# Performance work log

Hardware: AMD Instinct MI355X
Metric: run time of the kernel (lower is better)

Reference implementation:

```python
import jax, jax.numpy as jnp
import numpy as np


def _grid_neighbors(H, W):
    # 4-neighbor grid adjacency for the Mesh([H, W]) graph
    idx = np.arange(H * W).reshape(H, W)
    p = np.full((H + 2, W + 2), -1, dtype=np.int64)
    p[1:-1, 1:-1] = idx
    nbrs = np.stack([p[0:H, 1:W + 1], p[2:H + 2, 1:W + 1], p[1:H + 1, 0:W], p[1:H + 1, 2:W + 2]], axis=-1).reshape(H * W, 4)
    mask = (nbrs >= 0).astype(np.float32)
    return np.where(nbrs >= 0, nbrs, 0), mask, mask.sum(-1) + 1.0


def _conv(x, w, b):
    y = jax.lax.conv_general_dilated(x, w, (1, 1), 'SAME', dimension_numbers=('NCHW', 'OIHW', 'NCHW'))
    return y + b[None, :, None, None]


def _dconv(x, w1, b1, w2, b2):
    return jax.nn.relu(_conv(jax.nn.relu(_conv(x, w1, b1)), w2, b2))


def _maxpool(x):
    return jax.lax.reduce_window(x, -jnp.inf, jax.lax.max, (1, 1, 2, 2), (1, 1, 2, 2), 'VALID')


def _convT(x, w, b):
    # kernel=2, stride=2 transposed conv (non-overlapping upsample)
    y = jax.lax.conv_transpose(x, w, (2, 2), 'VALID', dimension_numbers=('NCHW', 'HWIO', 'NCHW'))
    return y + b[None, :, None, None]


def _gconv(X, W, b, nbrs, mask, deg):
    # mesh graph conv: D^-1 (A + I) X W, irregular gather over grid adjacency
    g = X[:, nbrs, :]                                          # [B, N, 4, C]
    agg = ((g * mask[None, :, :, None]).sum(2) + X) / deg[None, :, None]
    return jax.nn.relu(jnp.einsum('bnc,cd->bnd', agg, W) + b[None, None, :])


def _forward(x, d1w1, d1b1, d1w2, d1b2, d2w1, d2b1, d2w2, d2b2, md1w, md1b, md2w, md2b, mbw, mbb, mu1w, mu1b, mu2w, mu2b, u3tw, u3tb, u3w1, u3b1, u3w2, u3b2, u4tw, u4tb, u4w1, u4b1, u4w2, u4b2, ow, ob):
    b1 = _dconv(x, d1w1, d1b1, d1w2, d1b2)                     # [1,64,256,256]
    b2 = _dconv(_maxpool(b1), d2w1, d2b1, d2w2, d2b2)          # [1,128,128,128]
    fe = _maxpool(b2)                                           # [1,128,64,64]
    fe = jnp.pad(fe, ((0, 0), (0, 0), (1, 1), (1, 1)))          # pad -> 66x66
    B, C, Hm, Wm = fe.shape
    nbrs, mask, deg = _grid_neighbors(Hm, Wm)
    nbrs, mask, deg = jnp.asarray(nbrs), jnp.asarray(mask), jnp.asarray(deg)
    X = fe.reshape(B, C, Hm * Wm).transpose(0, 2, 1)            # [1, 4356, 128]
    bp1 = _gconv(X, md1w, md1b, nbrs, mask, deg)                # 256 (skip)
    bp2 = _gconv(bp1, md2w, md2b, nbrs, mask, deg)              # 512 (skip)
    Xb = _gconv(bp2, mbw, mbb, nbrs, mask, deg)                 # 1024 mesh bottleneck
    X = _gconv(Xb, mu1w, mu1b, nbrs, mask, deg) + bp2           # 512
    X = _gconv(X, mu2w, mu2b, nbrs, mask, deg) + bp1            # 256
    fe = X.transpose(0, 2, 1).reshape(B, 256, Hm, Wm)[:, :, 1:-1, 1:-1]  # unpad -> 64x64
    u3 = _convT(fe, u3tw, u3tb)                                 # [1,128,128,128]
    fe = _dconv(jnp.concatenate([b2, u3], 1), u3w1, u3b1, u3w2, u3b2)
    u4 = _convT(fe, u4tw, u4tb)                                 # [1,64,256,256]
    fe = _dconv(jnp.concatenate([b1, u4], 1), u4w1, u4b1, u4w2, u4b2)
    return _conv(fe, ow, ob)[:, 0]                              # [1,256,256]


def setup_inputs():
    ks = iter(jax.random.split(jax.random.key(0), 40))
    def W(shape, fan_in):
        return jax.random.normal(next(ks), shape, jnp.float32) * np.float32(np.sqrt(2.0 / fan_in))
    def Z(n):
        return jnp.zeros((n,), jnp.float32)
    return {
        'x': jax.random.normal(next(ks), (1, 3, 256, 256), jnp.float32),
        'd1w1': W((64, 3, 3, 3), 27), 'd1b1': Z(64), 'd1w2': W((64, 64, 3, 3), 576), 'd1b2': Z(64),
        'd2w1': W((128, 64, 3, 3), 576), 'd2b1': Z(128), 'd2w2': W((128, 128, 3, 3), 1152), 'd2b2': Z(128),
        'md1w': W((128, 256), 128), 'md1b': Z(256),
        'md2w': W((256, 512), 256), 'md2b': Z(512),
        'mbw': W((512, 1024), 512), 'mbb': Z(1024),
        'mu1w': W((1024, 512), 1024), 'mu1b': Z(512),
        'mu2w': W((512, 256), 512), 'mu2b': Z(256),
        'u3tw': W((2, 2, 256, 128), 1024), 'u3tb': Z(128),
        'u3w1': W((128, 256, 3, 3), 2304), 'u3b1': Z(128), 'u3w2': W((128, 128, 3, 3), 1152), 'u3b2': Z(128),
        'u4tw': W((2, 2, 128, 64), 512), 'u4tb': Z(64),
        'u4w1': W((64, 128, 3, 3), 1152), 'u4b1': Z(64), 'u4w2': W((64, 64, 3, 3), 576), 'u4b2': Z(64),
        'ow': W((1, 64, 3, 3), 576), 'ob': Z(1),
    }


def reference(x, d1w1, d1b1, d1w2, d1b2, d2w1, d2b1, d2w2, d2b2, md1w, md1b, md2w, md2b, mbw, mbb, mu1w, mu1b, mu2w, mu2b, u3tw, u3tb, u3w1, u3b1, u3w2, u3b2, u4tw, u4tb, u4w1, u4b1, u4w2, u4b2, ow, ob):
    return _forward(x, d1w1, d1b1, d1w2, d1b2, d2w1, d2b1, d2w2, d2b2, md1w, md1b, md2w, md2b, mbw, mbb, mu1w, mu1b, mu2w, mu2b, u3tw, u3tb, u3w1, u3b1, u3w2, u3b2, u4tw, u4tb, u4w1, u4b1, u4w2, u4b2, ow, ob)
```

## Files before the change

### kernel.cpp

```cpp
#include <hip/hip_runtime.h>
#include <cstddef>

#define TPB 256

typedef __attribute__((ext_vector_type(8))) short short8;
typedef __attribute__((ext_vector_type(4))) float f32x4;

__device__ inline unsigned short f2bf(float f) {
    unsigned int u = __builtin_bit_cast(unsigned int, f);
    u += 0x7fffu + ((u >> 16) & 1u);
    return (unsigned short)(u >> 16);
}
__device__ inline float bf2f(unsigned short h) {
    unsigned int u = ((unsigned int)h) << 16;
    return __builtin_bit_cast(float, u);
}

struct TapOffs { int o[9]; };

template<int KCW>
__global__ __launch_bounds__(TPB) void k_gemmS(
    const unsigned short* __restrict__ A0, const unsigned short* __restrict__ Wf,
    const float* __restrict__ bias, const unsigned short* __restrict__ resid,
    unsigned short* __restrict__ O0, int NTtot)
{
    constexpr int K = KCW * 128;
    __shared__ float red[12 * 4 * 64 * 4];
    int lane = threadIdx.x & 63, wave = threadIdx.x >> 6;
    int ml = lane & 15, kq = lane >> 4;
    int m0 = blockIdx.x * 64, nb = blockIdx.y;
    int N = NTtot * 16;

    const unsigned short* Ap[4];
    #pragma unroll
    for (int i = 0; i < 4; ++i) {
        int mf = (wave + i) & 3;
        Ap[i] = A0 + (size_t)(m0 + mf * 16 + ml) * K + wave * (KCW * 32) + kq * 8;
    }
    const unsigned short* Bp = Wf + ((size_t)(wave * KCW) * NTtot + nb * 4) * 512 + lane * 8;

    f32x4 acc[4][4];
    #pragma unroll
    for (int i = 0; i < 4; ++i)
        #pragma unroll
        for (int nt = 0; nt < 4; ++nt) acc[i][nt] = (f32x4){0.f, 0.f, 0.f, 0.f};

    #pragma unroll
    for (int q = 0; q < KCW; ++q) {
        short8 b[4];
        #pragma unroll
        for (int nt = 0; nt < 4; ++nt)
            b[nt] = *(const short8*)(Bp + ((size_t)q * NTtot + nt) * 512);
        short8 a[4];
        #pragma unroll
        for (int i = 0; i < 4; ++i)
            a[i] = *(const short8*)(Ap[i] + q * 32);
        #pragma unroll
        for (int i = 0; i < 4; ++i)
            #pragma unroll
            for (int nt = 0; nt < 4; ++nt)
                acc[i][nt] = __builtin_amdgcn_mfma_f32_16x16x32_bf16(a[i], b[nt], acc[i][nt], 0, 0, 0);
    }

    #pragma unroll
    for (int i = 1; i < 4; ++i) {
        int s = wave * 3 + (i - 1);
        #pragma unroll
        for (int nt = 0; nt < 4; ++nt)
            *(f32x4*)&red[(((s * 4 + nt) * 64) + lane) * 4] = acc[i][nt];
    }
    __syncthreads();
    #pragma unroll
    for (int w2 = 0; w2 < 4; ++w2) {
        if (w2 == wave) continue;
        int i = (wave - w2) & 3;
        int s = w2 * 3 + (i - 1);
        #pragma unroll
        for (int nt = 0; nt < 4; ++nt) {
            f32x4 v = *(const f32x4*)&red[(((s * 4 + nt) * 64) + lane) * 4];
            acc[0][nt] += v;
        }
    }

    int mrow = m0 + wave * 16 + kq * 4;
    unsigned short* Ot = O0 + (size_t)mrow * N + nb * 64;
    const unsigned short* Rt = resid ? resid + (size_t)mrow * N + nb * 64 : nullptr;
    #pragma unroll
    for (int nt = 0; nt < 4; ++nt) {
        float bv = bias[nb * 64 + nt * 16 + ml];
        #pragma unroll
        for (int r = 0; r < 4; ++r) {
            float v = fmaxf(acc[0][nt][r] + bv, 0.f);
            if (Rt) v += bf2f(Rt[(size_t)r * N + nt * 16 + ml]);
            Ot[(size_t)r * N + nt * 16 + ml] = f2bf(v);
        }
    }
}

template<int CHUNKS>
__global__ __launch_bounds__(TPB) void k_conv3g(
    const unsigned short* __restrict__ A0, const unsigned short* __restrict__ Wf,
    const float* __restrict__ bias, unsigned short* __restrict__ O0,
    int AP, int tilesX, int OMS, int OP, int NTtot)
{
    constexpr int Cs  = CHUNKS * 64;
    constexpr int KC2 = CHUNKS * 2;
    __shared__ unsigned short Bs[2][12288];

    int lane = threadIdx.x & 63, wave = threadIdx.x >> 6;
    int ml = lane & 15, kq = lane >> 4;
    int nb = blockIdx.y;
    int tileX = blockIdx.x % tilesX, tileY = blockIdx.x / tilesX;
    int gx0 = tileX * 64, gy = tileY * 4 + wave;

    const unsigned short* Abase = A0 + (size_t)(gy - 1) * AP
                                     + (size_t)(gx0 + ml - 1) * Cs + kq * 8;

    f32x4 acc[4][4];
    #pragma unroll
    for (int mf = 0; mf < 4; ++mf)
        #pragma unroll
        for (int nt = 0; nt < 4; ++nt) acc[mf][nt] = (f32x4){0.f, 0.f, 0.f, 0.f};

    const int G = CHUNKS * 3;

    auto stageB = [&](int g) {
        int ch = g / 3, ky = g - (g / 3) * 3;
        unsigned short* bd = Bs[g & 1];
        #pragma unroll
        for (int it = 0; it < 6; ++it) {
            int u = threadIdx.x + it * TPB;
            int e = u * 8;
            int kxq = e >> 11;
            int rem = e & 2047;
            int kx = kxq >> 1, q = kxq & 1;
            const unsigned short* src = Wf
                + ((size_t)((ky * 3 + kx) * KC2 + ch * 2 + q) * NTtot + nb * 4) * 512 + rem;
            *(int4*)&bd[e] = *(const int4*)src;
        }
    };

    stageB(0);
    __syncthreads();
    for (int g = 0; g < G; ++g) {
        if (g + 1 < G) stageB(g + 1);
        int ch = g / 3, ky = g - (g / 3) * 3;
        const unsigned short* Ar = Abase + (size_t)ky * AP + ch * 64;
        const unsigned short* Bb = &Bs[g & 1][lane * 8];
        #pragma unroll
        for (int kx = 0; kx < 3; ++kx) {
            #pragma unroll
            for (int q = 0; q < 2; ++q) {
                short8 b[4];
                #pragma unroll
                for (int nt = 0; nt < 4; ++nt)
                    b[nt] = *(const short8*)(Bb + (kx * 2 + q) * 2048 + nt * 512);
                short8 a[4];
                #pragma unroll
                for (int mf = 0; mf < 4; ++mf)
                    a[mf] = *(const short8*)(Ar + (size_t)(kx + mf * 16) * Cs + q * 32);
                #pragma unroll
                for (int mf = 0; mf < 4; ++mf)
                    #pragma unroll
                    for (int nt = 0; nt < 4; ++nt)
                        acc[mf][nt] = __builtin_amdgcn_mfma_f32_16x16x32_bf16(a[mf], b[nt], acc[mf][nt], 0, 0, 0);
            }
        }
        __syncthreads();
    }

    unsigned short* Orow = O0 + (size_t)gy * OP + (size_t)nb * 64;
    #pragma unroll
    for (int mf = 0; mf < 4; ++mf) {
        int gx = gx0 + mf * 16 + kq * 4;
        #pragma unroll
        for (int nt = 0; nt < 4; ++nt) {
            float bv = bias[nb * 64 + nt * 16 + ml];
            #pragma unroll
            for (int r = 0; r < 4; ++r) {
                float v = fmaxf(acc[mf][nt][r] + bv, 0.f);
                Orow[(size_t)(gx + r) * OMS + nt * 16 + ml] = f2bf(v);
            }
        }
    }
}

template<int MW, int KC>
__global__ __launch_bounds__(TPB) void k_gemm(
    const unsigned short* __restrict__ A0, const unsigned short* __restrict__ Wf,
    const float* __restrict__ bias, const unsigned short* __restrict__ resid, int RS,
    unsigned short* __restrict__ O0,
    int Cs, int AP, int Wimg, int OMS, int OP,
    int T, TapOffs toffs, int NTtot, int relu, int ct, int ctDy, int ctDx)
{
    int lane = threadIdx.x & 63, wave = threadIdx.x >> 6;
    int ml = lane & 15, kq = lane >> 4;
    int nb = blockIdx.y;

    const unsigned short* Wb = Wf;
    unsigned short* Ob = O0;
    if (ct) {
        int tp = blockIdx.z;
        Wb += (size_t)(tp * KC) * NTtot * 512;
        int dy = 1 - (tp >> 1), dx = 1 - (tp & 1);
        Ob += (size_t)dy * ctDy + (size_t)dx * ctDx;
    }
    const unsigned short* WbB = Wb + (size_t)(nb * 4) * 512 + lane * 8;

    int fy[MW], fx[MW];
    const unsigned short* Af[MW];
    #pragma unroll
    for (int f = 0; f < MW; ++f) {
        int mf = (blockIdx.x * 4 + wave) * (16 * MW) + f * 16;
        int y = mf / Wimg, x = mf - y * Wimg;
        fy[f] = y; fx[f] = x;
        Af[f] = A0 + (size_t)y * AP + (size_t)(x + ml) * Cs + kq * 8;
    }

    f32x4 acc[MW][4];
    #pragma unroll
    for (int f = 0; f < MW; ++f)
        #pragma unroll
        for (int nt = 0; nt < 4; ++nt) acc[f][nt] = (f32x4){0.f, 0.f, 0.f, 0.f};

    for (int tp = 0; tp < T; ++tp) {
        int toff = toffs.o[tp];
        const unsigned short* Wt = WbB + (size_t)(tp * KC) * NTtot * 512;
        #pragma unroll
        for (int q = 0; q < KC; ++q) {
            short8 b[4];
            #pragma unroll
            for (int nt = 0; nt < 4; ++nt)
                b[nt] = *(const short8*)(Wt + (size_t)q * NTtot * 512 + nt * 512);
            short8 a[MW];
            #pragma unroll
            for (int f = 0; f < MW; ++f)
                a[f] = *(const short8*)(Af[f] + toff + q * 32);
            #pragma unroll
            for (int f = 0; f < MW; ++f)
                #pragma unroll
                for (int nt = 0; nt < 4; ++nt)
                    acc[f][nt] = __builtin_amdgcn_mfma_f32_16x16x32_bf16(a[f], b[nt], acc[f][nt], 0, 0, 0);
        }
    }

    #pragma unroll
    for (int f = 0; f < MW; ++f) {
        unsigned short* Ot = Ob + (size_t)fy[f] * OP + (size_t)(fx[f] + kq * 4) * OMS + (size_t)nb * 64;
        int mg0 = (blockIdx.x * 4 + wave) * (16 * MW) + f * 16 + kq * 4;
        #pragma unroll
        for (int nt = 0; nt < 4; ++nt) {
            int ng = nb * 64 + nt * 16 + ml;
            float bv = bias[ng];
            #pragma unroll
            for (int r = 0; r < 4; ++r) {
                float v = acc[f][nt][r] + bv;
                if (relu) v = fmaxf(v, 0.f);
                if (resid) v += bf2f(resid[(size_t)(mg0 + r) * RS + ng]);
                Ot[(size_t)r * OMS + nt * 16 + ml] = f2bf(v);
            }
        }
    }
}

struct PackArgs {
    const float* w[15];
    int cum[16];
    int mode[15], KC[15], NT[15], K[15], N[15];
};
__global__ __launch_bounds__(TPB) void k_pack_all(
    PackArgs pa, unsigned short* __restrict__ dst, int total)
{
    int idx = blockIdx.x * TPB + threadIdx.x;
    if (idx >= total) return;
    int e = 0;
    #pragma unroll
    for (int i = 1; i < 15; ++i) e += (idx >= pa.cum[i]);
    int local = idx - pa.cum[e];
    const float* w = pa.w[e];
    int KC = pa.KC[e], NT = pa.NT[e], K = pa.K[e], N = pa.N[e], mode = pa.mode[e];

    int j = local & 7, l = (local >> 3) & 63;
    int r = local >> 9;
    int ntg = r % NT; int r2 = r / NT;
    int q = r2 % KC; int tp = r2 / KC;
    int k = q * 32 + (l >> 4) * 8 + j;
    int n = ntg * 16 + (l & 15);
    float v = 0.f;
    if (mode == 0) { int ky = tp / 3, kx = tp % 3; v = w[(size_t)(n * K + k) * 9 + ky * 3 + kx]; }
    else if (mode == 1) { v = w[(size_t)k * N + n]; }
    else if (mode == 2) { v = w[((size_t)tp * K + k) * N + n]; }
    else { if (k < 27) { int tap = k / 3, c = k % 3; int ky = tap / 3, kx = tap % 3;
                         v = w[((n * 3 + c) * 3 + ky) * 3 + kx]; } }
    dst[idx] = f2bf(v);
}

struct ZArgs { int off[10]; int cum[11]; int W2[10]; int H2[10]; int Cs[10]; };
__global__ __launch_bounds__(TPB) void k_zero_all(
    ZArgs za, unsigned short* __restrict__ W, int total)
{
    int idx = blockIdx.x * TPB + threadIdx.x;
    if (idx >= total) return;
    int e = 0;
    #pragma unroll
    for (int i = 1; i < 10; ++i) e += (idx >= za.cum[i]);
    int local = idx - za.cum[e];
    int W2 = za.W2[e], H2 = za.H2[e], Cs = za.Cs[e];
    int topbot = 2 * W2 * Cs;
    int iy, ix, c;
    if (local < topbot) {
        int row = local / (W2 * Cs); int rest = local - row * (W2 * Cs);
        iy = row ? (H2 - 1) : 0; ix = rest / Cs; c = rest - (rest / Cs) * Cs;
    } else {
        int idx2 = local - topbot;
        int per = (H2 - 2) * Cs;
        int side = idx2 / per; int rest = idx2 - side * per;
        iy = 1 + rest / Cs; ix = side ? (W2 - 1) : 0; c = rest - (rest / Cs) * Cs;
    }
    W[(size_t)za.off[e] + ((size_t)iy * W2 + ix) * Cs + c] = 0;
}

__global__ __launch_bounds__(TPB) void k_im2col(
    const float* __restrict__ x, unsigned short* __restrict__ xcol)
{
    int idx = blockIdx.x * TPB + threadIdx.x;
    if (idx >= 65536 * 32) return;
    int k = idx & 31, m = idx >> 5;
    int y = m >> 8, xx = m & 255;
    float v = 0.f;
    if (k < 27) {
        int tap = k / 3, c = k - tap * 3;
        int ty = tap / 3, tx = tap % 3;
        int yy = y + ty - 1, xp = xx + tx - 1;
        if (yy >= 0 && yy < 256 && xp >= 0 && xp < 256)
            v = x[c * 65536 + yy * 256 + xp];
    }
    xcol[idx] = f2bf(v);
}

__global__ __launch_bounds__(TPB) void k_maxpool(
    const unsigned short* __restrict__ inI, unsigned short* __restrict__ outI,
    int Wo, int C4, int CsIn, int inPitch, int CsOut, int outPitch, int total)
{
    int idx = blockIdx.x * TPB + threadIdx.x;
    if (idx >= total) return;
    int c4 = idx % C4; int p = idx / C4;
    int x = p % Wo, y = p / Wo;
    const unsigned short* ip = inI + (size_t)(2 * y) * inPitch + (size_t)(2 * x) * CsIn + c4 * 4;
    ushort4 a = *(const ushort4*)(ip);
    ushort4 b = *(const ushort4*)(ip + CsIn);
    ushort4 c = *(const ushort4*)(ip + inPitch);
    ushort4 d = *(const ushort4*)(ip + inPitch + CsIn);
    ushort4 o;
    o.x = f2bf(fmaxf(fmaxf(bf2f(a.x), bf2f(b.x)), fmaxf(bf2f(c.x), bf2f(d.x))));
    o.y = f2bf(fmaxf(fmaxf(bf2f(a.y), bf2f(b.y)), fmaxf(bf2f(c.y), bf2f(d.y))));
    o.z = f2bf(fmaxf(fmaxf(bf2f(a.z), bf2f(b.z)), fmaxf(bf2f(c.z), bf2f(d.z))));
    o.w = f2bf(fmaxf(fmaxf(bf2f(a.w), bf2f(b.w)), fmaxf(bf2f(c.w), bf2f(d.w))));
    *(ushort4*)(outI + (size_t)y * outPitch + (size_t)x * CsOut + c4 * 4) = o;
}

__global__ __launch_bounds__(TPB) void k_gagg(
    const unsigned short* __restrict__ X, unsigned short* __restrict__ agg,
    int C, int total)
{
    int idx = blockIdx.x * TPB + threadIdx.x;
    if (idx >= total) return;
    int C4 = C >> 2;
    int c4 = idx % C4; int n = idx / C4;
    int i = n / 66, j = n - i * 66;
    size_t base = (size_t)n * C + c4 * 4;
    ushort4 s = *(const ushort4*)(X + base);
    float v0 = bf2f(s.x), v1 = bf2f(s.y), v2 = bf2f(s.z), v3 = bf2f(s.w);
    float cnt = 1.f;
    if (i > 0)  { ushort4 u = *(const ushort4*)(X + base - (size_t)66 * C);
                  v0 += bf2f(u.x); v1 += bf2f(u.y); v2 += bf2f(u.z); v3 += bf2f(u.w); cnt += 1.f; }
    if (i < 65) { ushort4 u = *(const ushort4*)(X + base + (size_t)66 * C);
                  v0 += bf2f(u.x); v1 += bf2f(u.y); v2 += bf2f(u.z); v3 += bf2f(u.w); cnt += 1.f; }
    if (j > 0)  { ushort4 u = *(const ushort4*)(X + base - C);
                  v0 += bf2f(u.x); v1 += bf2f(u.y); v2 += bf2f(u.z); v3 += bf2f(u.w); cnt += 1.f; }
    if (j < 65) { ushort4 u = *(const ushort4*)(X + base + C);
                  v0 += bf2f(u.x); v1 += bf2f(u.y); v2 += bf2f(u.z); v3 += bf2f(u.w); cnt += 1.f; }
    float inv = 1.f / cnt;
    ushort4 o;
    o.x = f2bf(v0 * inv); o.y = f2bf(v1 * inv); o.z = f2bf(v2 * inv); o.w = f2bf(v3 * inv);
    *(ushort4*)(agg + base) = o;
}

__global__ __launch_bounds__(TPB) void k_outconv(
    const unsigned short* __restrict__ vI, const float* __restrict__ ow,
    const float* __restrict__ ob, float* __restrict__ out)
{
    __shared__ float wl[576];
    for (int i = threadIdx.x; i < 576; i += TPB) wl[i] = ow[i];
    __syncthreads();
    int p = blockIdx.x * TPB + threadIdx.x;
    int y = p >> 8, x = p & 255;
    float acc = ob[0];
    #pragma unroll
    for (int ky = 0; ky < 3; ++ky)
        #pragma unroll
        for (int kx = 0; kx < 3; ++kx) {
            const unsigned short* ip = vI + (size_t)((y + ky - 1) * 258 + (x + kx - 1)) * 64;
            int wb = ky * 3 + kx;
            for (int c = 0; c < 64; c += 4) {
                ushort4 uv = *(const ushort4*)(ip + c);
                acc += bf2f(uv.x) * wl[c * 9 + wb] + bf2f(uv.y) * wl[(c + 1) * 9 + wb]
                     + bf2f(uv.z) * wl[(c + 2) * 9 + wb] + bf2f(uv.w) * wl[(c + 3) * 9 + wb];
            }
        }
    out[p] = acc;
}

static inline TapOffs zero_toffs() { TapOffs t = {}; return t; }

extern "C" void kernel_launch(void* const* d_in, const int* in_sizes, int n_in,
                              void* d_out, int out_size, void* d_ws, size_t ws_size,
                              hipStream_t stream) {
    const float* x    = (const float*)d_in[0];
    const float* d1w1 = (const float*)d_in[1];  const float* d1b1 = (const float*)d_in[2];
    const float* d1w2 = (const float*)d_in[3];  const float* d1b2 = (const float*)d_in[4];
    const float* d2w1 = (const float*)d_in[5];  const float* d2b1 = (const float*)d_in[6];
    const float* d2w2 = (const float*)d_in[7];  const float* d2b2 = (const float*)d_in[8];
    const float* md1w = (const float*)d_in[9];  const float* md1b = (const float*)d_in[10];
    const float* md2w = (const float*)d_in[11]; const float* md2b = (const float*)d_in[12];
    const float* mbw  = (const float*)d_in[13]; const float* mbb  = (const float*)d_in[14];
    const float* mu1w = (const float*)d_in[15]; const float* mu1b = (const float*)d_in[16];
    const float* mu2w = (const float*)d_in[17]; const float* mu2b = (const float*)d_in[18];
    const float* u3tw = (const float*)d_in[19]; const float* u3tb = (const float*)d_in[20];
    const float* u3w1 = (const float*)d_in[21]; const float* u3b1 = (const float*)d_in[22];
    const float* u3w2 = (const float*)d_in[23]; const float* u3b2 = (const float*)d_in[24];
    const float* u4tw = (const float*)d_in[25]; const float* u4tb = (const float*)d_in[26];
    const float* u4w1 = (const float*)d_in[27]; const float* u4b1 = (const float*)d_in[28];
    const float* u4w2 = (const float*)d_in[29]; const float* u4b2 = (const float*)d_in[30];
    const float* ow   = (const float*)d_in[31]; const float* ob   = (const float*)d_in[32];
    float* out = (float*)d_out;

    unsigned short* W = (unsigned short*)d_ws;

    const size_t XCOL = 0;
    const size_t A1   = 2097152;
    const size_t CAT4 = 6357248;
    const size_t P1   = 14877440;
    const size_t T2   = 15959040;
    const size_t CAT3 = 18122240;
    const size_t X0   = 22448640;
    const size_t BP1  = 23006208;
    const size_t BP2  = 24185856;
    const size_t XB   = 26545152;
    const size_t XC   = 31263744;
    const size_t XD   = 33623040;
    const size_t V3A  = 34802688;
    const size_t V3B  = 36965888;
    const size_t V4A  = 39129088;
    const size_t V4B  = 43389184;
    const size_t AGG  = 47649280;
    const size_t WP   = 52367872;

    const size_t a1I   = A1 + 259 * 64;
    const size_t cat4I = CAT4 + 259 * 128;
    const size_t p1I   = P1 + 131 * 64;
    const size_t t2I   = T2 + 131 * 128;
    const size_t cat3I = CAT3 + 131 * 256;
    const size_t X0I   = X0 + 67 * 128;
    const size_t XdI   = XD + 67 * 256;
    const size_t v3aI  = V3A + 131 * 128;
    const size_t v3bI  = V3B + 131 * 128;
    const size_t v4aI  = V4A + 259 * 64;
    const size_t v4bI  = V4B + 259 * 64;

    dim3 blk(TPB);
    const int BIG = 1 << 28;

    {
        ZArgs za;
        const int off[10] = {(int)A1,(int)CAT4,(int)P1,(int)T2,(int)CAT3,(int)V3A,(int)V3B,(int)V4A,(int)V4B,(int)X0};
        const int w2 [10] = {258,258,130,130,130,130,130,258,258,66};
        const int h2 [10] = {258,258,130,130,130,130,130,258,258,66};
        const int cs [10] = {64,128,64,128,256,128,128,64,64,128};
        int cum = 0;
        for (int i = 0; i < 10; ++i) {
            za.off[i]=off[i]; za.W2[i]=w2[i]; za.H2[i]=h2[i]; za.Cs[i]=cs[i];
            za.cum[i]=cum; cum += (w2[i]*h2[i] - (w2[i]-2)*(h2[i]-2))*cs[i];
        }
        za.cum[10]=cum;
        k_zero_all<<<dim3((cum + TPB - 1) / TPB), blk, 0, stream>>>(za, W, cum);
    }

    {
        PackArgs pa;
        const float* ws_[15] = {d1w1,d1w2,d2w1,d2w2,md1w,md2w,mbw,mu1w,mu2w,u3tw,u3w1,u3w2,u4tw,u4w1,u4w2};
        const int mode[15] = {3,0,0,0,1,1,1,1,1,2,0,0,2,0,0};
        const int kc [15] = {1,2,2,4,4,8,16,32,16,8,8,4,4,4,2};
        const int nt [15] = {4,4,8,8,16,32,64,32,16,8,8,8,4,4,4};
        const int kk [15] = {32,64,64,128,128,256,512,1024,512,256,256,128,128,128,64};
        const int nn [15] = {64,64,128,128,256,512,1024,512,256,128,128,128,64,64,64};
        const int tt [15] = {1,9,9,9,1,1,1,1,1,4,9,9,4,9,9};
        int cum = 0;
        for (int i = 0; i < 15; ++i) {
            pa.w[i]=ws_[i]; pa.mode[i]=mode[i]; pa.KC[i]=kc[i]; pa.NT[i]=nt[i];
            pa.K[i]=kk[i]; pa.N[i]=nn[i]; pa.cum[i]=cum;
            cum += tt[i]*kc[i]*nt[i]*512;
        }
        pa.cum[15]=cum;
        k_pack_all<<<dim3((cum + TPB - 1) / TPB), blk, 0, stream>>>(pa, W + WP, cum);
    }
    const size_t pw_d1w1=WP+0, pw_d1w2=WP+2048, pw_d2w1=WP+38912, pw_d2w2=WP+112640,
        pw_md1=WP+260096, pw_md2=WP+292864, pw_mb=WP+423936, pw_mu1=WP+948224,
        pw_mu2=WP+1472512, pw_u3t=WP+1603584, pw_u3w1=WP+1734656, pw_u3w2=WP+2029568,
        pw_u4t=WP+2177024, pw_u4w1=WP+2209792, pw_u4w2=WP+2283520;

    k_im2col<<<dim3(8192), blk, 0, stream>>>(x, W + XCOL);
    k_gemm<2,1><<<dim3(512,1), blk, 0, stream>>>(W + XCOL, W + pw_d1w1, d1b1, nullptr, 0,
        W + a1I, 32, 8192, 256, 64, 258*64, 1, zero_toffs(), 4, 1, 0,0,0);
    k_conv3g<1><<<dim3(256,1), blk, 0, stream>>>(W + a1I, W + pw_d1w2, d1b2,
        W + cat4I, 258*64, 4, 128, 258*128, 4);
    k_maxpool<<<dim3(1024), blk, 0, stream>>>(W + cat4I, W + p1I, 128, 16, 128, 258*128, 64, 130*64, 128*128*16);
    k_conv3g<1><<<dim3(64,2), blk, 0, stream>>>(W + p1I, W + pw_d2w1, d2b1,
        W + t2I, 130*64, 2, 128, 130*128, 8);
    k_conv3g<2><<<dim3(64,2), blk, 0, stream>>>(W + t2I, W + pw_d2w2, d2b2,
        W + cat3I, 130*128, 2, 256, 130*256, 8);
    k_maxpool<<<dim3(512), blk, 0, stream>>>(W + cat3I, W + X0I, 64, 32, 256, 130*256, 128, 66*128, 64*64*32);

    k_gagg<<<dim3(545), blk, 0, stream>>>(W + X0, W + AGG, 128, 4356*32);
    k_gemmS<1><<<dim3(72,4), blk, 0, stream>>>(W + AGG, W + pw_md1, md1b, nullptr, W + BP1, 16);
    k_gagg<<<dim3(1089), blk, 0, stream>>>(W + BP1, W + AGG, 256, 4356*64);
    k_gemmS<2><<<dim3(72,8), blk, 0, stream>>>(W + AGG, W + pw_md2, md2b, nullptr, W + BP2, 32);
    k_gagg<<<dim3(2178), blk, 0, stream>>>(W + BP2, W + AGG, 512, 4356*128);
    k_gemmS<4><<<dim3(72,16), blk, 0, stream>>>(W + AGG, W + pw_mb, mbb, nullptr, W + XB, 64);
    k_gagg<<<dim3(4356), blk, 0, stream>>>(W + XB, W + AGG, 1024, 4356*256);
    k_gemmS<8><<<dim3(72,8), blk, 0, stream>>>(W + AGG, W + pw_mu1, mu1b, W + BP2, W + XC, 32);
    k_gagg<<<dim3(2178), blk, 0, stream>>>(W + XC, W + AGG, 512, 4356*128);
    k_gemmS<4><<<dim3(72,4), blk, 0, stream>>>(W + AGG, W + pw_mu2, mu2b, W + BP1, W + XD, 16);

    k_gemm<2,8><<<dim3(32,2,4), blk, 0, stream>>>(W + XdI, W + pw_u3t, u3tb, nullptr, 0,
        W + cat3I + 128, 256, 66*256, 64, 512, 2*130*256, 1, zero_toffs(), 8, 0, 1, 130*256, 256);
    k_conv3g<4><<<dim3(64,2), blk, 0, stream>>>(W + cat3I, W + pw_u3w1, u3b1,
        W + v3aI, 130*256, 2, 128, 130*128, 8);
    k_conv3g<2><<<dim3(64,2), blk, 0, stream>>>(W + v3aI, W + pw_u3w2, u3b2,
        W + v3bI, 130*128, 2, 128, 130*128, 8);

    k_gemm<2,4><<<dim3(128,1,4), blk, 0, stream>>>(W + v3bI, W + pw_u4t, u4tb, nullptr, 0,
        W + cat4I + 64, 128, 130*128, 128, 256, 2*258*128, 1, zero_toffs(), 4, 0, 1, 258*128, 128);
    k_conv3g<2><<<dim3(256,1), blk, 0, stream>>>(W + cat4I, W + pw_u4w1, u4b1,
        W + v4aI, 258*128, 4, 64, 258*64, 4);
    k_conv3g<1><<<dim3(256,1), blk, 0, stream>>>(W + v4aI, W + pw_u4w2, u4b2,
        W + v4bI, 258*64, 4, 64, 258*64, 4);

    k_outconv<<<dim3(256), blk, 0, stream>>>(W + v4bI, ow, ob, out);
}
```

Baseline: 445.6 us.

## Shrink conv tiles to one output row per block, split-K transposed convs

Replaces the 4-row conv3g kernel with conv3f, where each block computes a single output row of 64 pixels and each wave handles 16 pixels. It stages weights per tap instead of per channel-chunk/ky group, which gives four times more blocks. The u3 transposed conv now uses the split-K gemmS kernel, extended with strided output and ct support, and the u4 transposed conv uses a new single-fragment gemmN kernel. The aim is higher occupancy and better wave parallelism on the small feature maps. The cost is less A-operand reuse per wave and more redundant weight staging per output.

```diff
diff --git a/kernel.cpp b/kernel.cpp
--- a/kernel.cpp
+++ b/kernel.cpp
@@ -18,26 +18,116 @@
 
 struct TapOffs { int o[9]; };
 
+template<int CHUNKS>
+__global__ __launch_bounds__(TPB) void k_conv3f(
+    const unsigned short* __restrict__ A0, const unsigned short* __restrict__ Wf,
+    const float* __restrict__ bias, unsigned short* __restrict__ O0,
+    int AP, int tilesX, int OMS, int OP, int NTtot)
+{
+    constexpr int Cs  = CHUNKS * 64;
+    constexpr int KC2 = CHUNKS * 2;
+    __shared__ unsigned short Bs[2][CHUNKS * 4096];
+
+    int lane = threadIdx.x & 63, wave = threadIdx.x >> 6;
+    int ml = lane & 15, kq = lane >> 4;
+    int nb = blockIdx.y;
+    int tileX = blockIdx.x % tilesX, gy = blockIdx.x / tilesX;
+    int gx0 = tileX * 64 + wave * 16;
+
+    const unsigned short* Abase = A0 + (size_t)(gy - 1) * AP
+                                     + (size_t)(gx0 + ml - 1) * Cs + kq * 8;
+
+    f32x4 acc[4];
+    #pragma unroll
+    for (int nt = 0; nt < 4; ++nt) acc[nt] = (f32x4){0.f, 0.f, 0.f, 0.f};
+
+    auto stageB = [&](int tap, int buf) {
+        unsigned short* bd = Bs[buf];
+        #pragma unroll
+        for (int it = 0; it < CHUNKS * 2; ++it) {
+            int u = threadIdx.x + it * TPB;
+            int e = u * 8;
+            int ch = e >> 12;
+            int rem = e & 4095;
+            int q = rem >> 11;
+            int rem2 = rem & 2047;
+            int ntg = rem2 >> 9;
+            int r = rem2 & 511;
+            const unsigned short* src = Wf
+                + ((size_t)(tap * KC2 + ch * 2 + q) * NTtot + nb * 4 + ntg) * 512 + r;
+            *(int4*)&bd[e] = *(const int4*)src;
+        }
+    };
+
+    stageB(0, 0);
+    __syncthreads();
+    #pragma unroll
+    for (int tap = 0; tap < 9; ++tap) {
+        if (tap < 8) stageB(tap + 1, (tap + 1) & 1);
+        int ky = tap / 3, kx = tap - (tap / 3) * 3;
+        const unsigned short* Ar = Abase + (size_t)ky * AP + kx * Cs;
+        const unsigned short* Bb = &Bs[tap & 1][lane * 8];
+        #pragma unroll
+        for (int ch = 0; ch < CHUNKS; ++ch) {
+            #pragma unroll
+            for (int q = 0; q < 2; ++q) {
+                short8 b[4];
+                #pragma unroll
+                for (int nt = 0; nt < 4; ++nt)
+                    b[nt] = *(const short8*)(Bb + ch * 4096 + q * 2048 + nt * 512);
+                short8 a = *(const short8*)(Ar + ch * 64 + q * 32);
+                #pragma unroll
+                for (int nt = 0; nt < 4; ++nt)
+                    acc[nt] = __builtin_amdgcn_mfma_f32_16x16x32_bf16(a, b[nt], acc[nt], 0, 0, 0);
+            }
+        }
+        __syncthreads();
+    }
+
+    unsigned short* Orow = O0 + (size_t)gy * OP + (size_t)nb * 64;
+    int gx = gx0 + kq * 4;
+    #pragma unroll
+    for (int nt = 0; nt < 4; ++nt) {
+        float bv = bias[nb * 64 + nt * 16 + ml];
+        #pragma unroll
+        for (int r = 0; r < 4; ++r) {
+            float v = fmaxf(acc[nt][r] + bv, 0.f);
+            Orow[(size_t)(gx + r) * OMS + nt * 16 + ml] = f2bf(v);
+        }
+    }
+}
+
 template<int KCW>
 __global__ __launch_bounds__(TPB) void k_gemmS(
     const unsigned short* __restrict__ A0, const unsigned short* __restrict__ Wf,
     const float* __restrict__ bias, const unsigned short* __restrict__ resid,
-    unsigned short* __restrict__ O0, int NTtot)
+    unsigned short* __restrict__ O0, int NTtot,
+    int AP, int Wimg, int OMS, int OP, int relu, int ct, int ctDy, int ctDx)
 {
     constexpr int K = KCW * 128;
     __shared__ float red[12 * 4 * 64 * 4];
     int lane = threadIdx.x & 63, wave = threadIdx.x >> 6;
     int ml = lane & 15, kq = lane >> 4;
     int m0 = blockIdx.x * 64, nb = blockIdx.y;
-    int N = NTtot * 16;
+
+    const unsigned short* Wb = Wf;
+    unsigned short* Ob = O0;
+    if (ct) {
+        int tp = blockIdx.z;
+        Wb += (size_t)(tp * KCW * 4) * NTtot * 512;
+        int dy = 1 - (tp >> 1), dx = 1 - (tp & 1);
+        Ob += (size_t)dy * ctDy + (size_t)dx * ctDx;
+    }
 
     const unsigned short* Ap[4];
     #pragma unroll
     for (int i = 0; i < 4; ++i) {
         int mf = (wave + i) & 3;
-        Ap[i] = A0 + (size_t)(m0 + mf * 16 + ml) * K + wave * (KCW * 32) + kq * 8;
-    }
-    const unsigned short* Bp = Wf + ((size_t)(wave * KCW) * NTtot + nb * 4) * 512 + lane * 8;
+        int m = m0 + mf * 16;
+        int y = m / Wimg, x = m - y * Wimg;
+        Ap[i] = A0 + (size_t)y * AP + (size_t)(x + ml) * K + wave * (KCW * 32) + kq * 8;
+    }
+    const unsigned short* Bp = Wb + ((size_t)(wave * KCW) * NTtot + nb * 4) * 512 + lane * 8;
 
     f32x4 acc[4][4];
     #pragma unroll
@@ -83,115 +173,28 @@
     }
 
     int mrow = m0 + wave * 16 + kq * 4;
-    unsigned short* Ot = O0 + (size_t)mrow * N + nb * 64;
-    const unsigned short* Rt = resid ? resid + (size_t)mrow * N + nb * 64 : nullptr;
+    int y = mrow / Wimg, x = mrow - y * Wimg;
+    unsigned short* Ot = Ob + (size_t)y * OP + (size_t)x * OMS + nb * 64;
+    const unsigned short* Rt = resid ? resid + (size_t)mrow * OMS + nb * 64 : nullptr;
     #pragma unroll
     for (int nt = 0; nt < 4; ++nt) {
         float bv = bias[nb * 64 + nt * 16 + ml];
         #pragma unroll
         for (int r = 0; r < 4; ++r) {
-            float v = fmaxf(acc[0][nt][r] + bv, 0.f);
-            if (Rt) v += bf2f(Rt[(size_t)r * N + nt * 16 + ml]);
-            Ot[(size_t)r * N + nt * 16 + ml] = f2bf(v);
-        }
-    }
-}
-
-template<int CHUNKS>
-__global__ __launch_bounds__(TPB) void k_conv3g(
+            float v = acc[0][nt][r] + bv;
+            if (relu) v = fmaxf(v, 0.f);
+            if (Rt) v += bf2f(Rt[(size_t)r * OMS + nt * 16 + ml]);
+            Ot[(size_t)r * OMS + nt * 16 + ml] = f2bf(v);
+        }
+    }
+}
+
+template<int KC>
+__global__ __launch_bounds__(TPB) void k_gemmN(
     const unsigned short* __restrict__ A0, const unsigned short* __restrict__ Wf,
     const float* __restrict__ bias, unsigned short* __restrict__ O0,
-    int AP, int tilesX, int OMS, int OP, int NTtot)
-{
-    constexpr int Cs  = CHUNKS * 64;
-    constexpr int KC2 = CHUNKS * 2;
-    __shared__ unsigned short Bs[2][12288];
-
-    int lane = threadIdx.x & 63, wave = threadIdx.x >> 6;
-    int ml = lane & 15, kq = lane >> 4;
-    int nb = blockIdx.y;
-    int tileX = blockIdx.x % tilesX, tileY = blockIdx.x / tilesX;
-    int gx0 = tileX * 64, gy = tileY * 4 + wave;
-
-    const unsigned short* Abase = A0 + (size_t)(gy - 1) * AP
-                                     + (size_t)(gx0 + ml - 1) * Cs + kq * 8;
-
-    f32x4 acc[4][4];
-    #pragma unroll
-    for (int mf = 0; mf < 4; ++mf)
-        #pragma unroll
-        for (int nt = 0; nt < 4; ++nt) acc[mf][nt] = (f32x4){0.f, 0.f, 0.f, 0.f};
-
-    const int G = CHUNKS * 3;
-
-    auto stageB = [&](int g) {
-        int ch = g / 3, ky = g - (g / 3) * 3;
-        unsigned short* bd = Bs[g & 1];
-        #pragma unroll
-        for (int it = 0; it < 6; ++it) {
-            int u = threadIdx.x + it * TPB;
-            int e = u * 8;
-            int kxq = e >> 11;
-            int rem = e & 2047;
-            int kx = kxq >> 1, q = kxq & 1;
-            const unsigned short* src = Wf
-                + ((size_t)((ky * 3 + kx) * KC2 + ch * 2 + q) * NTtot + nb * 4) * 512 + rem;
-            *(int4*)&bd[e] = *(const int4*)src;
-        }
-    };
-
-    stageB(0);
-    __syncthreads();
-    for (int g = 0; g < G; ++g) {
-        if (g + 1 < G) stageB(g + 1);
-        int ch = g / 3, ky = g - (g / 3) * 3;
-        const unsigned short* Ar = Abase + (size_t)ky * AP + ch * 64;
-        const unsigned short* Bb = &Bs[g & 1][lane * 8];
-        #pragma unroll
-        for (int kx = 0; kx < 3; ++kx) {
-            #pragma unroll
-            for (int q = 0; q < 2; ++q) {
-                short8 b[4];
-                #pragma unroll
-                for (int nt = 0; nt < 4; ++nt)
-                    b[nt] = *(const short8*)(Bb + (kx * 2 + q) * 2048 + nt * 512);
-                short8 a[4];
-                #pragma unroll
-                for (int mf = 0; mf < 4; ++mf)
-                    a[mf] = *(const short8*)(Ar + (size_t)(kx + mf * 16) * Cs + q * 32);
-                #pragma unroll
-                for (int mf = 0; mf < 4; ++mf)
-                    #pragma unroll
-                    for (int nt = 0; nt < 4; ++nt)
-                        acc[mf][nt] = __builtin_amdgcn_mfma_f32_16x16x32_bf16(a[mf], b[nt], acc[mf][nt], 0, 0, 0);
-            }
-        }
-        __syncthreads();
-    }
-
-    unsigned short* Orow = O0 + (size_t)gy * OP + (size_t)nb * 64;
-    #pragma unroll
-    for (int mf = 0; mf < 4; ++mf) {
-        int gx = gx0 + mf * 16 + kq * 4;
-        #pragma unroll
-        for (int nt = 0; nt < 4; ++nt) {
-            float bv = bias[nb * 64 + nt * 16 + ml];
-            #pragma unroll
-            for (int r = 0; r < 4; ++r) {
-                float v = fmaxf(acc[mf][nt][r] + bv, 0.f);
-                Orow[(size_t)(gx + r) * OMS + nt * 16 + ml] = f2bf(v);
-            }
-        }
-    }
-}
-
-template<int MW, int KC>
-__global__ __launch_bounds__(TPB) void k_gemm(
-    const unsigned short* __restrict__ A0, const unsigned short* __restrict__ Wf,
-    const float* __restrict__ bias, const unsigned short* __restrict__ resid, int RS,
-    unsigned short* __restrict__ O0,
-    int Cs, int AP, int Wimg, int OMS, int OP,
-    int T, TapOffs toffs, int NTtot, int relu, int ct, int ctDy, int ctDx)
+    int Cs, int AP, int Wimg, int OMS, int OP, int NTtot, int relu,
+    int ct, int ctDy, int ctDx)
 {
     int lane = threadIdx.x & 63, wave = threadIdx.x >> 6;
     int ml = lane & 15, kq = lane >> 4;
@@ -205,7 +208,51 @@
         int dy = 1 - (tp >> 1), dx = 1 - (tp & 1);
         Ob += (size_t)dy * ctDy + (size_t)dx * ctDx;
     }
-    const unsigned short* WbB = Wb + (size_t)(nb * 4) * 512 + lane * 8;
+    int m0 = blockIdx.x * 64 + wave * 16;
+    int y = m0 / Wimg, x = m0 - y * Wimg;
+    const unsigned short* Arow = A0 + (size_t)y * AP + (size_t)(x + ml) * Cs + kq * 8;
+    const unsigned short* Bp = Wb + (size_t)(nb * 4) * 512 + lane * 8;
+
+    f32x4 acc[4];
+    #pragma unroll
+    for (int nt = 0; nt < 4; ++nt) acc[nt] = (f32x4){0.f, 0.f, 0.f, 0.f};
+
+    #pragma unroll
+    for (int q = 0; q < KC; ++q) {
+        short8 b[4];
+        #pragma unroll
+        for (int nt = 0; nt < 4; ++nt)
+            b[nt] = *(const short8*)(Bp + ((size_t)q * NTtot + nt) * 512);
+        short8 a = *(const short8*)(Arow + q * 32);
+        #pragma unroll
+        for (int nt = 0; nt < 4; ++nt)
+            acc[nt] = __builtin_amdgcn_mfma_f32_16x16x32_bf16(a, b[nt], acc[nt], 0, 0, 0);
+    }
+
+    unsigned short* Ot = Ob + (size_t)y * OP + (size_t)(x + kq * 4) * OMS + (size_t)nb * 64;
+    #pragma unroll
+    for (int nt = 0; nt < 4; ++nt) {
+        float bv = bias[nb * 64 + nt * 16 + ml];
+        #pragma unroll
+        for (int r = 0; r < 4; ++r) {
+            float v = acc[nt][r] + bv;
+            if (relu) v = fmaxf(v, 0.f);
+            Ot[(size_t)r * OMS + nt * 16 + ml] = f2bf(v);
+        }
+    }
+}
+
+template<int MW, int KC>
+__global__ __launch_bounds__(TPB) void k_gemm(
+    const unsigned short* __restrict__ A0, const unsigned short* __restrict__ Wf,
+    const float* __restrict__ bias, unsigned short* __restrict__ O0,
+    int Cs, int AP, int Wimg, int OMS, int OP,
+    int T, TapOffs toffs, int NTtot, int relu)
+{
+    int lane = threadIdx.x & 63, wave = threadIdx.x >> 6;
+    int ml = lane & 15, kq = lane >> 4;
+    int nb = blockIdx.y;
+    const unsigned short* WbB = Wf + (size_t)(nb * 4) * 512 + lane * 8;
 
     int fy[MW], fx[MW];
     const unsigned short* Af[MW];
@@ -246,17 +293,14 @@
 
     #pragma unroll
     for (int f = 0; f < MW; ++f) {
-        unsigned short* Ot = Ob + (size_t)fy[f] * OP + (size_t)(fx[f] + kq * 4) * OMS + (size_t)nb * 64;
-        int mg0 = (blockIdx.x * 4 + wave) * (16 * MW) + f * 16 + kq * 4;
+        unsigned short* Ot = O0 + (size_t)fy[f] * OP + (size_t)(fx[f] + kq * 4) * OMS + (size_t)nb * 64;
         #pragma unroll
         for (int nt = 0; nt < 4; ++nt) {
-            int ng = nb * 64 + nt * 16 + ml;
-            float bv = bias[ng];
+            float bv = bias[nb * 64 + nt * 16 + ml];
             #pragma unroll
             for (int r = 0; r < 4; ++r) {
                 float v = acc[f][nt][r] + bv;
                 if (relu) v = fmaxf(v, 0.f);
-                if (resid) v += bf2f(resid[(size_t)(mg0 + r) * RS + ng]);
                 Ot[(size_t)r * OMS + nt * 16 + ml] = f2bf(v);
             }
         }
@@ -510,40 +554,45 @@
         pw_u4t=WP+2177024, pw_u4w1=WP+2209792, pw_u4w2=WP+2283520;
 
     k_im2col<<<dim3(8192), blk, 0, stream>>>(x, W + XCOL);
-    k_gemm<2,1><<<dim3(512,1), blk, 0, stream>>>(W + XCOL, W + pw_d1w1, d1b1, nullptr, 0,
-        W + a1I, 32, 8192, 256, 64, 258*64, 1, zero_toffs(), 4, 1, 0,0,0);
-    k_conv3g<1><<<dim3(256,1), blk, 0, stream>>>(W + a1I, W + pw_d1w2, d1b2,
+    k_gemm<2,1><<<dim3(512,1), blk, 0, stream>>>(W + XCOL, W + pw_d1w1, d1b1,
+        W + a1I, 32, 8192, 256, 64, 258*64, 1, zero_toffs(), 4, 1);
+    k_conv3f<1><<<dim3(1024,1), blk, 0, stream>>>(W + a1I, W + pw_d1w2, d1b2,
         W + cat4I, 258*64, 4, 128, 258*128, 4);
     k_maxpool<<<dim3(1024), blk, 0, stream>>>(W + cat4I, W + p1I, 128, 16, 128, 258*128, 64, 130*64, 128*128*16);
-    k_conv3g<1><<<dim3(64,2), blk, 0, stream>>>(W + p1I, W + pw_d2w1, d2b1,
+    k_conv3f<1><<<dim3(256,2), blk, 0, stream>>>(W + p1I, W + pw_d2w1, d2b1,
         W + t2I, 130*64, 2, 128, 130*128, 8);
-    k_conv3g<2><<<dim3(64,2), blk, 0, stream>>>(W + t2I, W + pw_d2w2, d2b2,
+    k_conv3f<2><<<dim3(256,2), blk, 0, stream>>>(W + t2I, W + pw_d2w2, d2b2,
         W + cat3I, 130*128, 2, 256, 130*256, 8);
     k_maxpool<<<dim3(512), blk, 0, stream>>>(W + cat3I, W + X0I, 64, 32, 256, 130*256, 128, 66*128, 64*64*32);
 
     k_gagg<<<dim3(545), blk, 0, stream>>>(W + X0, W + AGG, 128, 4356*32);
-    k_gemmS<1><<<dim3(72,4), blk, 0, stream>>>(W + AGG, W + pw_md1, md1b, nullptr, W + BP1, 16);
+    k_gemmS<1><<<dim3(72,4), blk, 0, stream>>>(W + AGG, W + pw_md1, md1b, nullptr,
+        W + BP1, 16, 0, BIG, 256, 0, 1, 0, 0, 0);
     k_gagg<<<dim3(1089), blk, 0, stream>>>(W + BP1, W + AGG, 256, 4356*64);
-    k_gemmS<2><<<dim3(72,8), blk, 0, stream>>>(W + AGG, W + pw_md2, md2b, nullptr, W + BP2, 32);
+    k_gemmS<2><<<dim3(72,8), blk, 0, stream>>>(W + AGG, W + pw_md2, md2b, nullptr,
+        W + BP2, 32, 0, BIG, 512, 0, 1, 0, 0, 0);
     k_gagg<<<dim3(2178), blk, 0, stream>>>(W + BP2, W + AGG, 512, 4356*128);
-    k_gemmS<4><<<dim3(72,16), blk, 0, stream>>>(W + AGG, W + pw_mb, mbb, nullptr, W + XB, 64);
+    k_gemmS<4><<<dim3(72,16), blk, 0, stream>>>(W + AGG, W + pw_mb, mbb, nullptr,
+        W + XB, 64, 0, BIG, 1024, 0, 1, 0, 0, 0);
     k_gagg<<<dim3(4356), blk, 0, stream>>>(W + XB, W + AGG, 1024, 4356*256);
-    k_gemmS<8><<<dim3(72,8), blk, 0, stream>>>(W + AGG, W + pw_mu1, mu1b, W + BP2, W + XC, 32);
+    k_gemmS<8><<<dim3(72,8), blk, 0, stream>>>(W + AGG, W + pw_mu1, mu1b, W + BP2,
+        W + XC, 32, 0, BIG, 512, 0, 1, 0, 0, 0);
     k_gagg<<<dim3(2178), blk, 0, stream>>>(W + XC, W + AGG, 512, 4356*128);
-    k_gemmS<4><<<dim3(72,4), blk, 0, stream>>>(W + AGG, W + pw_mu2, mu2b, W + BP1, W + XD, 16);
-
-    k_gemm<2,8><<<dim3(32,2,4), blk, 0, stream>>>(W + XdI, W + pw_u3t, u3tb, nullptr, 0,
-        W + cat3I + 128, 256, 66*256, 64, 512, 2*130*256, 1, zero_toffs(), 8, 0, 1, 130*256, 256);
-    k_conv3g<4><<<dim3(64,2), blk, 0, stream>>>(W + cat3I, W + pw_u3w1, u3b1,
+    k_gemmS<4><<<dim3(72,4), blk, 0, stream>>>(W + AGG, W + pw_mu2, mu2b, W + BP1,
+        W + XD, 16, 0, BIG, 256, 0, 1, 0, 0, 0);
+
+    k_gemmS<2><<<dim3(64,2,4), blk, 0, stream>>>(W + XdI, W + pw_u3t, u3tb, nullptr,
+        W + cat3I + 128, 8, 66*256, 64, 512, 2*130*256, 0, 1, 130*256, 256);
+    k_conv3f<4><<<dim3(256,2), blk, 0, stream>>>(W + cat3I, W + pw_u3w1, u3b1,
         W + v3aI, 130*256, 2, 128, 130*128, 8);
-    k_conv3g<2><<<dim3(64,2), blk, 0, stream>>>(W + v3aI, W + pw_u3w2, u3b2,
+    k_conv3f<2><<<dim3(256,2), blk, 0, stream>>>(W + v3aI, W + pw_u3w2, u3b2,
         W + v3bI, 130*128, 2, 128, 130*128, 8);
 
-    k_gemm<2,4><<<dim3(128,1,4), blk, 0, stream>>>(W + v3bI, W + pw_u4t, u4tb, nullptr, 0,
-        W + cat4I + 64, 128, 130*128, 128, 256, 2*258*128, 1, zero_toffs(), 4, 0, 1, 258*128, 128);
-    k_conv3g<2><<<dim3(256,1), blk, 0, stream>>>(W + cat4I, W + pw_u4w1, u4b1,
+    k_gemmN<4><<<dim3(256,1,4), blk, 0, stream>>>(W + v3bI, W + pw_u4t, u4tb,
+        W + cat4I + 64, 128, 130*128, 128, 256, 2*258*128, 4, 0, 1, 258*128, 128);
+    k_conv3f<2><<<dim3(1024,1), blk, 0, stream>>>(W + cat4I, W + pw_u4w1, u4b1,
         W + v4aI, 258*128, 4, 64, 258*64, 4);
-    k_conv3g<1><<<dim3(256,1), blk, 0, stream>>>(W + v4aI, W + pw_u4w2, u4b2,
+    k_conv3f<1><<<dim3(1024,1), blk, 0, stream>>>(W + v4aI, W + pw_u4w2, u4b2,
         W + v4bI, 258*64, 4, 64, 258*64, 4);
 
     k_outconv<<<dim3(256), blk, 0, stream>>>(W + v4bI, ow, ob, out);
```

Result: faster. 396.2 us (-11.1%).
